# Optimization experiments

Measured on AMD Instinct MI355X. Metric: run time of the kernel, lower is better.

## Reference

```python
import jax, jax.numpy as jnp
import numpy as np

EPS = 1e-12

def setup_inputs() -> dict:
    key = jax.random.key(0)
    k1, k2, k3, k4 = jax.random.split(key, 4)
    N_TABLE, N_NODES, N_SAMP, D_IN, D_OUT = 200000, 50000, 32, 256, 256
    features = jax.random.normal(k1, (N_TABLE, D_IN), dtype=jnp.float32)
    node_idx = jax.random.randint(k2, (N_NODES,), 0, N_TABLE)
    neigh_idx = jax.random.randint(k3, (N_NODES, N_SAMP), 0, N_TABLE)
    W = jax.random.normal(k4, (D_IN, D_OUT), dtype=jnp.float32) / np.sqrt(D_IN)
    b = jnp.zeros((D_OUT,), dtype=jnp.float32)
    return {"node_idx": node_idx, "neigh_idx": neigh_idx, "features": features, "W": W, "b": b}

def reference(node_idx, neigh_idx, features, W, b):
    # MeanAggregator with self_loop: mean over sampled neighbors + the node itself
    n_samp = neigh_idx.shape[1]
    neigh_feats = features[neigh_idx]            # [N, S, D] gather
    self_feats = features[node_idx]              # [N, D]
    agg = (neigh_feats.sum(axis=1) + self_feats) / (n_samp + 1)  # [N, D]
    # Combine: linear -> ReLU activation -> L2 normalize
    out = jax.nn.relu(agg @ W + b)               # [N, D_out]
    norm = jnp.sqrt(jnp.sum(out * out, axis=-1, keepdims=True))
    out = out / jnp.maximum(norm, EPS)
    return out
```

## Files before the change

kernel.cpp:

```cpp
#include <hip/hip_runtime.h>
#include <hip/hip_bf16.h>

typedef __attribute__((ext_vector_type(8))) short short8;
typedef __attribute__((ext_vector_type(4))) float f32x4;

#define D_IN   256
#define D_OUT  256
#define NSAMP  32

static __device__ __forceinline__ unsigned short f2bf(float f) {
    unsigned int u = __builtin_bit_cast(unsigned int, f);
    u += 0x7fffu + ((u >> 16) & 1u);
    return (unsigned short)(u >> 16);
}

static __device__ __forceinline__ void accum8(float* a, uint4 v) {
    a[0] += __builtin_bit_cast(float, v.x << 16);
    a[1] += __builtin_bit_cast(float, v.x & 0xffff0000u);
    a[2] += __builtin_bit_cast(float, v.y << 16);
    a[3] += __builtin_bit_cast(float, v.y & 0xffff0000u);
    a[4] += __builtin_bit_cast(float, v.z << 16);
    a[5] += __builtin_bit_cast(float, v.z & 0xffff0000u);
    a[6] += __builtin_bit_cast(float, v.w << 16);
    a[7] += __builtin_bit_cast(float, v.w & 0xffff0000u);
}

__global__ void wconv_kernel(const float* __restrict__ W,
                             unsigned short* __restrict__ wsw) {
    const int k = blockIdx.x;
    const int n = threadIdx.x;
    const float v = W[k * D_OUT + n];
    const int ks = k >> 5, kg = (k >> 3) & 3, j = k & 7;
    const int nf = n >> 4, c = n & 15;
    const int lane = kg * 16 + c;
    const int dst = ((ks * 16 + nf) * 64 + lane) * 8 + j;
    wsw[dst] = f2bf(v);
}

__global__ __launch_bounds__(256, 4) void ygemm_kernel(
        const float* __restrict__ feat,
        const unsigned short* __restrict__ wsw,
        unsigned short* __restrict__ Y,
        int n_table)
{
    __shared__ __attribute__((aligned(16))) unsigned char lds[64 * 512];

    const int tid  = threadIdx.x;
    const int wv   = tid >> 6;
    const int lane = tid & 63;
    const int row0 = blockIdx.x * 64;

    const int r = tid >> 2;
    const int q = tid & 3;
    #pragma unroll 4
    for (int it = 0; it < 16; ++it) {
        const int cidx = it * 4 + q;
        const int grow = row0 + r;
        float4 f = make_float4(0.f, 0.f, 0.f, 0.f);
        if (grow < n_table)
            f = *(const float4*)(feat + (size_t)grow * D_IN + cidx * 4);
        ushort4 pk;
        pk.x = f2bf(f.x); pk.y = f2bf(f.y); pk.z = f2bf(f.z); pk.w = f2bf(f.w);
        unsigned int bo = (unsigned int)(r * 512 + cidx * 8) ^ ((unsigned int)(r & 7) << 4);
        *(ushort4*)(&lds[bo]) = pk;
    }
    __syncthreads();

    f32x4 acc[16];
    #pragma unroll
    for (int i = 0; i < 16; ++i) acc[i] = (f32x4)(0.0f);

    const int arow = wv * 16 + (lane & 15);
    const int acol = (lane >> 4) * 16;
    const short8* __restrict__ wp = (const short8*)wsw;

    #pragma unroll
    for (int ks = 0; ks < 8; ++ks) {
        unsigned int bo = (unsigned int)(arow * 512 + ks * 64 + acol)
                        ^ ((unsigned int)(arow & 7) << 4);
        const short8 afrag = *(const short8*)(&lds[bo]);
        #pragma unroll
        for (int nf = 0; nf < 16; ++nf) {
            const short8 bfrag = wp[(ks * 16 + nf) * 64 + lane];
            acc[nf] = __builtin_amdgcn_mfma_f32_16x16x32_bf16(afrag, bfrag, acc[nf], 0, 0, 0);
        }
    }

    const int rbase = row0 + wv * 16 + (lane >> 4) * 4;
    const int c0 = lane & 15;
    #pragma unroll
    for (int j = 0; j < 4; ++j) {
        const int rg = rbase + j;
        if (rg < n_table) {
            #pragma unroll
            for (int nf = 0; nf < 16; ++nf)
                Y[(size_t)rg * D_OUT + nf * 16 + c0] = f2bf(acc[nf][j]);
        }
    }
}

__global__ __launch_bounds__(256) void gather_kernel(
        const int*  __restrict__ node_idx,
        const int*  __restrict__ neigh_idx,
        const unsigned short* __restrict__ Y,
        const float* __restrict__ bias,
        float* __restrict__ out,
        int n_nodes)
{
    const int tid  = threadIdx.x;
    const int l    = tid & 31;
    const int node = blockIdx.x * 8 + (tid >> 5);
    const bool valid = node < n_nodes;

    const int nb   = valid ? neigh_idx[node * NSAMP + l] : 0;
    const int sidx = valid ? node_idx[node] : 0;

    float a[8] = {0.f, 0.f, 0.f, 0.f, 0.f, 0.f, 0.f, 0.f};

    #pragma unroll 8
    for (int s = 0; s < NSAMP; ++s) {
        const int idx = __shfl(nb, s, 32);
        const uint4 v = *(const uint4*)(Y + (size_t)idx * D_OUT + l * 8);
        accum8(a, v);
    }
    {
        const uint4 v = *(const uint4*)(Y + (size_t)sidx * D_OUT + l * 8);
        accum8(a, v);
    }

    const float sc = 1.0f / (float)(NSAMP + 1);
    const float4 b0 = *(const float4*)(bias + l * 8);
    const float4 b1 = *(const float4*)(bias + l * 8 + 4);
    float o[8];
    o[0] = fmaxf(a[0] * sc + b0.x, 0.f);
    o[1] = fmaxf(a[1] * sc + b0.y, 0.f);
    o[2] = fmaxf(a[2] * sc + b0.z, 0.f);
    o[3] = fmaxf(a[3] * sc + b0.w, 0.f);
    o[4] = fmaxf(a[4] * sc + b1.x, 0.f);
    o[5] = fmaxf(a[5] * sc + b1.y, 0.f);
    o[6] = fmaxf(a[6] * sc + b1.z, 0.f);
    o[7] = fmaxf(a[7] * sc + b1.w, 0.f);

    float p = 0.f;
    #pragma unroll
    for (int j = 0; j < 8; ++j) p += o[j] * o[j];
    #pragma unroll
    for (int m = 1; m < 32; m <<= 1) p += __shfl_xor(p, m, 64);
    const float inv = 1.0f / fmaxf(sqrtf(p), 1e-12f);

    if (valid) {
        float4 s0, s1;
        s0.x = o[0] * inv; s0.y = o[1] * inv; s0.z = o[2] * inv; s0.w = o[3] * inv;
        s1.x = o[4] * inv; s1.y = o[5] * inv; s1.z = o[6] * inv; s1.w = o[7] * inv;
        float* op = out + (size_t)node * D_OUT + l * 8;
        *(float4*)op       = s0;
        *(float4*)(op + 4) = s1;
    }
}

__global__ __launch_bounds__(256, 4) void gcn_fused_kernel(
        const int*  __restrict__ node_idx,
        const int*  __restrict__ neigh_idx,
        const float* __restrict__ features,
        const unsigned short* __restrict__ wsw,
        const float* __restrict__ bias,
        float* __restrict__ out,
        int n_nodes)
{
    __shared__ __attribute__((aligned(16))) unsigned char lds[64 * D_IN * 2];

    const int tid  = threadIdx.x;
    const int wv   = tid >> 6;
    const int lane = tid & 63;
    const int block_m0 = blockIdx.x * 64;

    const float scale = 1.0f / (float)(NSAMP + 1);
    for (int r = 0; r < 16; ++r) {
        const int row  = wv * 16 + r;
        const int node = block_m0 + row;
        float ax = 0.f, ay = 0.f, az = 0.f, aw = 0.f;
        if (node < n_nodes) {
            const int nb   = neigh_idx[node * NSAMP + (lane & 31)];
            const int self = node_idx[node];
            {
                const float4 v = *(const float4*)(features + (size_t)self * D_IN + lane * 4);
                ax += v.x; ay += v.y; az += v.z; aw += v.w;
            }
            #pragma unroll 8
            for (int s = 0; s < NSAMP; ++s) {
                const int idx = __shfl(nb, s, 64);
                const float4 v = *(const float4*)(features + (size_t)idx * D_IN + lane * 4);
                ax += v.x; ay += v.y; az += v.z; aw += v.w;
            }
            ax *= scale; ay *= scale; az *= scale; aw *= scale;
        }
        ushort4 pk;
        pk.x = f2bf(ax); pk.y = f2bf(ay); pk.z = f2bf(az); pk.w = f2bf(aw);
        unsigned int bo = (unsigned int)(row * 512 + lane * 8) ^ ((unsigned int)(row & 7) << 4);
        *(ushort4*)(&lds[bo]) = pk;
    }
    __syncthreads();

    f32x4 acc[16];
    #pragma unroll
    for (int i = 0; i < 16; ++i) acc[i] = (f32x4)(0.0f);

    const int arow = wv * 16 + (lane & 15);
    const int acol = (lane >> 4) * 16;
    const short8* __restrict__ wp = (const short8*)wsw;

    #pragma unroll
    for (int ks = 0; ks < 8; ++ks) {
        unsigned int bo = (unsigned int)(arow * 512 + ks * 64 + acol)
                        ^ ((unsigned int)(arow & 7) << 4);
        const short8 afrag = *(const short8*)(&lds[bo]);
        #pragma unroll
        for (int nf = 0; nf < 16; ++nf) {
            const short8 bfrag = wp[(ks * 16 + nf) * 64 + lane];
            acc[nf] = __builtin_amdgcn_mfma_f32_16x16x32_bf16(afrag, bfrag, acc[nf], 0, 0, 0);
        }
    }

    float p[4] = {0.f, 0.f, 0.f, 0.f};
    #pragma unroll
    for (int nf = 0; nf < 16; ++nf) {
        const float bv = bias[nf * 16 + (lane & 15)];
        #pragma unroll
        for (int j = 0; j < 4; ++j) {
            float v = acc[nf][j] + bv;
            v = fmaxf(v, 0.0f);
            acc[nf][j] = v;
            p[j] += v * v;
        }
    }
    #pragma unroll
    for (int m = 1; m < 16; m <<= 1) {
        p[0] += __shfl_xor(p[0], m, 64);
        p[1] += __shfl_xor(p[1], m, 64);
        p[2] += __shfl_xor(p[2], m, 64);
        p[3] += __shfl_xor(p[3], m, 64);
    }
    float inv[4];
    #pragma unroll
    for (int j = 0; j < 4; ++j)
        inv[j] = 1.0f / fmaxf(sqrtf(p[j]), 1e-12f);

    const int rbase = block_m0 + wv * 16 + (lane >> 4) * 4;
    const int c0 = lane & 15;
    #pragma unroll
    for (int j = 0; j < 4; ++j) {
        const int rg = rbase + j;
        if (rg < n_nodes) {
            #pragma unroll
            for (int nf = 0; nf < 16; ++nf)
                out[(size_t)rg * D_OUT + nf * 16 + c0] = acc[nf][j] * inv[j];
        }
    }
}

extern "C" void kernel_launch(void* const* d_in, const int* in_sizes, int n_in,
                              void* d_out, int out_size, void* d_ws, size_t ws_size,
                              hipStream_t stream) {
    const int*   node_idx  = (const int*)d_in[0];
    const int*   neigh_idx = (const int*)d_in[1];
    const float* features  = (const float*)d_in[2];
    const float* W         = (const float*)d_in[3];
    const float* bias      = (const float*)d_in[4];
    float*       out       = (float*)d_out;
    const int n_nodes = in_sizes[0];
    const int n_table = in_sizes[2] / D_IN;

    unsigned short* wsw = (unsigned short*)d_ws;
    unsigned short* Y   = (unsigned short*)((char*)d_ws + 131072);

    const size_t need = 131072 + (size_t)n_table * D_OUT * 2;

    hipLaunchKernelGGL(wconv_kernel, dim3(D_IN), dim3(D_OUT), 0, stream, W, wsw);

    if (ws_size >= need) {
        const int yblocks = (n_table + 63) / 64;
        hipLaunchKernelGGL(ygemm_kernel, dim3(yblocks), dim3(256), 0, stream,
                           features, wsw, Y, n_table);
        const int gblocks = (n_nodes + 7) / 8;
        hipLaunchKernelGGL(gather_kernel, dim3(gblocks), dim3(256), 0, stream,
                           node_idx, neigh_idx, Y, bias, out, n_nodes);
    } else {
        const int nblocks = (n_nodes + 63) / 64;
        hipLaunchKernelGGL(gcn_fused_kernel, dim3(nblocks), dim3(256), 0, stream,
                           node_idx, neigh_idx, features, wsw, bias, out, n_nodes);
    }
}
```

Baseline: 528.2 us.

## Load GEMM A fragments directly from global and use persistent wave tiling

The Y-GEMM kernel no longer stages the feature tile through LDS with a block barrier. Each wave now loads its own 16-row A fragments straight from global memory, converts them to bf16 in registers, and loops over 16-row tiles in a grid-stride fashion on a fixed 2048-block grid. This removes the LDS writes, the swizzled reads and the __syncthreads. In exchange, the global A loads are less coalesced: each lane reads 32 bytes per row per k-step. The direct loads also have no explicit staging to hide their latency.

After: 1.060 ms. 101% more time.

```diff
diff --git a/kernel.cpp b/kernel.cpp
--- a/kernel.cpp
+++ b/kernel.cpp
@@ -43,58 +43,56 @@
         unsigned short* __restrict__ Y,
         int n_table)
 {
-    __shared__ __attribute__((aligned(16))) unsigned char lds[64 * 512];
-
     const int tid  = threadIdx.x;
     const int wv   = tid >> 6;
     const int lane = tid & 63;
-    const int row0 = blockIdx.x * 64;
-
-    const int r = tid >> 2;
-    const int q = tid & 3;
-    #pragma unroll 4
-    for (int it = 0; it < 16; ++it) {
-        const int cidx = it * 4 + q;
-        const int grow = row0 + r;
-        float4 f = make_float4(0.f, 0.f, 0.f, 0.f);
-        if (grow < n_table)
-            f = *(const float4*)(feat + (size_t)grow * D_IN + cidx * 4);
-        ushort4 pk;
-        pk.x = f2bf(f.x); pk.y = f2bf(f.y); pk.z = f2bf(f.z); pk.w = f2bf(f.w);
-        unsigned int bo = (unsigned int)(r * 512 + cidx * 8) ^ ((unsigned int)(r & 7) << 4);
-        *(ushort4*)(&lds[bo]) = pk;
-    }
-    __syncthreads();
-
-    f32x4 acc[16];
-    #pragma unroll
-    for (int i = 0; i < 16; ++i) acc[i] = (f32x4)(0.0f);
-
-    const int arow = wv * 16 + (lane & 15);
-    const int acol = (lane >> 4) * 16;
     const short8* __restrict__ wp = (const short8*)wsw;
 
-    #pragma unroll
-    for (int ks = 0; ks < 8; ++ks) {
-        unsigned int bo = (unsigned int)(arow * 512 + ks * 64 + acol)
-                        ^ ((unsigned int)(arow & 7) << 4);
-        const short8 afrag = *(const short8*)(&lds[bo]);
-        #pragma unroll
-        for (int nf = 0; nf < 16; ++nf) {
-            const short8 bfrag = wp[(ks * 16 + nf) * 64 + lane];
-            acc[nf] = __builtin_amdgcn_mfma_f32_16x16x32_bf16(afrag, bfrag, acc[nf], 0, 0, 0);
-        }
-    }
-
-    const int rbase = row0 + wv * 16 + (lane >> 4) * 4;
-    const int c0 = lane & 15;
-    #pragma unroll
-    for (int j = 0; j < 4; ++j) {
-        const int rg = rbase + j;
-        if (rg < n_table) {
+    const int ntiles = (n_table + 15) >> 4;
+    const int wave_id = blockIdx.x * 4 + wv;
+    const int nwaves  = gridDim.x * 4;
+
+    const int arow_l  = lane & 15;
+    const int akoff   = (lane >> 4) * 8;
+
+    for (int t = wave_id; t < ntiles; t += nwaves) {
+        const int row0 = t << 4;
+
+        f32x4 acc[16];
+        #pragma unroll
+        for (int i = 0; i < 16; ++i) acc[i] = (f32x4)(0.0f);
+
+        int ar = row0 + arow_l;
+        if (ar > n_table - 1) ar = n_table - 1;
+        const float* __restrict__ arow = feat + (size_t)ar * D_IN + akoff;
+
+        #pragma unroll
+        for (int ks = 0; ks < 8; ++ks) {
+            const float4 a0 = *(const float4*)(arow + ks * 32);
+            const float4 a1 = *(const float4*)(arow + ks * 32 + 4);
+            short8 af;
+            af[0] = (short)f2bf(a0.x); af[1] = (short)f2bf(a0.y);
+            af[2] = (short)f2bf(a0.z); af[3] = (short)f2bf(a0.w);
+            af[4] = (short)f2bf(a1.x); af[5] = (short)f2bf(a1.y);
+            af[6] = (short)f2bf(a1.z); af[7] = (short)f2bf(a1.w);
             #pragma unroll
-            for (int nf = 0; nf < 16; ++nf)
-                Y[(size_t)rg * D_OUT + nf * 16 + c0] = f2bf(acc[nf][j]);
+            for (int nf = 0; nf < 16; ++nf) {
+                const short8 bfrag = wp[(ks * 16 + nf) * 64 + lane];
+                acc[nf] = __builtin_amdgcn_mfma_f32_16x16x32_bf16(af, bfrag, acc[nf], 0, 0, 0);
+            }
+        }
+
+        const int c0 = lane & 15;
+        const int rbase = row0 + (lane >> 4) * 4;
+        #pragma unroll
+        for (int j = 0; j < 4; ++j) {
+            const int rg = rbase + j;
+            if (rg < n_table) {
+                unsigned short* yr = Y + (size_t)rg * D_OUT + c0;
+                #pragma unroll
+                for (int nf = 0; nf < 16; ++nf)
+                    yr[nf * 16] = f2bf(acc[nf][j]);
+            }
         }
     }
 }
@@ -278,8 +276,7 @@
     hipLaunchKernelGGL(wconv_kernel, dim3(D_IN), dim3(D_OUT), 0, stream, W, wsw);
 
     if (ws_size >= need) {
-        const int yblocks = (n_table + 63) / 64;
-        hipLaunchKernelGGL(ygemm_kernel, dim3(yblocks), dim3(256), 0, stream,
+        hipLaunchKernelGGL(ygemm_kernel, dim3(2048), dim3(256), 0, stream,
                            features, wsw, Y, n_table);
         const int gblocks = (n_nodes + 7) / 8;
         hipLaunchKernelGGL(gather_kernel, dim3(gblocks), dim3(256), 0, stream,
```
